# Kernel optimization log

Measured on AMD Instinct MI355X. Metric: run time of the kernel, lower is better.

The kernel has to match this reference:

```python
import jax, jax.numpy as jnp
import numpy as np

NUM_ENTITIES = 100000
NUM_RELATIONS = 500
D = 256            # embedding_dim
T = 4              # num_hash_tables
H = 32             # hash_dim
B = 64             # batch of queries
K = 10
CAND = max(K * 10, int(NUM_ENTITIES * 0.1))  # = 10000


def setup_inputs() -> dict:
    key = jax.random.key(0)
    k0, k1, k2, k3, k4 = jax.random.split(key, 5)
    return {
        "head": jax.random.randint(k0, (B,), 0, NUM_ENTITIES),
        "relation": jax.random.randint(k1, (B,), 0, NUM_RELATIONS),
        "entity_emb": jax.random.normal(k2, (NUM_ENTITIES, D), jnp.float32) * 0.02,
        "relation_emb": jax.random.normal(k3, (NUM_RELATIONS, D), jnp.float32) * 0.02,
        "hash_proj": jax.random.normal(k4, (T, D, H), jnp.float32),
        "k": K,
    }


def reference(head, relation, entity_emb, relation_emb, hash_proj, k):
    # DistMult approximate query path of KnowledgeGraph.query (use_approximate=True).
    h = entity_emb[head]            # [B, D]
    r = relation_emb[relation]      # [B, D]
    target = h * r                  # DistMult target embedding [B, D]

    # LSH hash codes (0/1 floats): projected > 0
    thash = (jnp.einsum('bd,tdh->bth', target, hash_proj) > 0).astype(jnp.float32)      # [B,T,H]
    ahash = (jnp.einsum('nd,tdh->nth', entity_emb, hash_proj) > 0).astype(jnp.float32)  # [N,T,H]

    # Hamming distance over (T,H) bits without materializing [B,N,T,H]:
    # mismatches = sum(a) + sum(b) - 2 * <a,b>  for 0/1 codes
    dot = jnp.einsum('bth,nth->bn', thash, ahash)                                        # [B,N]
    hash_dist = thash.sum((1, 2))[:, None] + ahash.sum((1, 2))[None, :] - 2.0 * dot      # [B,N]

    # top num_candidates with SMALLEST hamming distance
    _, cand_idx = jax.lax.top_k(-hash_dist, CAND)                                        # [B,CAND]

    # DistMult score: (h*r*t).sum(-1) == target . t ; compute dense then gather candidates
    scores_all = jnp.einsum('bd,nd->bn', target, entity_emb)                             # [B,N]
    cand_scores = jnp.take_along_axis(scores_all, cand_idx, axis=1)                      # [B,CAND]

    top_scores, top_local = jax.lax.top_k(cand_scores, k)                                # [B,k]
    top_indices = jnp.take_along_axis(cand_idx, top_local, axis=1)                       # [B,k]
    return top_indices, top_scores
```

## Files before the change

### kernel.cpp

```cpp
#include <hip/hip_runtime.h>
#include <hip/hip_bf16.h>
#include <float.h>

constexpr int NENT  = 100000;
constexpr int DDIM  = 256;
constexpr int BQ    = 64;
constexpr int CANDN = 10000;
constexpr int KTOP  = 10;
constexpr int NSLICE = 16;
constexpr int SLICE  = 6272;
constexpr int HPAD   = 132;

typedef short v8s __attribute__((ext_vector_type(8)));
typedef float v4f __attribute__((ext_vector_type(4)));

__device__ inline void split3(float x, unsigned short& h0, unsigned short& h1,
                              unsigned short& h2) {
    unsigned t0 = __float_as_uint(x) & 0xffff0000u;
    float r1 = x - __uint_as_float(t0);
    unsigned t1 = __float_as_uint(r1) & 0xffff0000u;
    float r2 = r1 - __uint_as_float(t1);
    h0 = (unsigned short)(t0 >> 16);
    h1 = (unsigned short)(t1 >> 16);
    h2 = (unsigned short)(__float_as_uint(r2) >> 16);
}

__device__ inline void split8p(const float* p0, const float* p1,
                               v8s& o0, v8s& o1, v8s& o2) {
    union { v8s v; unsigned short u[8]; } r0, r1, r2;
    float4 f0 = *(const float4*)p0;
    float4 f1 = *(const float4*)(p1);
    float av[8] = {f0.x, f0.y, f0.z, f0.w, f1.x, f1.y, f1.z, f1.w};
    #pragma unroll
    for (int j = 0; j < 8; j++)
        split3(av[j], r0.u[j], r1.u[j], r2.u[j]);
    o0 = r0.v; o1 = r1.v; o2 = r2.v;
}

__device__ inline void stage16(const float* g, float* l) {
    __builtin_amdgcn_global_load_lds(
        (const __attribute__((address_space(1))) void*)g,
        (__attribute__((address_space(3))) void*)l, 16, 0, 0);
}

__global__ __launch_bounds__(128) void k_targets(
    const int* __restrict__ head, const int* __restrict__ rel,
    const float* __restrict__ E, const float* __restrict__ Rm,
    const float* __restrict__ proj,
    float* __restrict__ tgtT, unsigned* __restrict__ thash)
{
    __shared__ float tg[DDIM];
    int b = blockIdx.x;
    int tid = threadIdx.x;
    int h = head[b], r = rel[b];
    for (int d = tid; d < DDIM; d += 128) {
        float v = E[h*DDIM + d] * Rm[r*DDIM + d];
        tg[d] = v;
        tgtT[d*BQ + b] = v;
    }
    __syncthreads();
    int t = tid >> 5, hh = tid & 31;
    float acc = 0.f;
    #pragma unroll 8
    for (int d = 0; d < DDIM; d++)
        acc += tg[d] * proj[(t*DDIM + d)*32 + hh];
    unsigned long long m = __ballot(acc > 0.0f);
    int lane = tid & 63, w = tid >> 6;
    if (lane == 0) {
        thash[b*4 + w*2 + 0] = (unsigned)(m & 0xffffffffull);
        thash[b*4 + w*2 + 1] = (unsigned)(m >> 32);
    }
}

__global__ __launch_bounds__(256) void k_prepw(
    const float* __restrict__ proj, const float* __restrict__ tgtT,
    unsigned short* __restrict__ Whi, unsigned short* __restrict__ Wmid,
    unsigned short* __restrict__ Wlo)
{
    int c = blockIdx.x;
    int d = threadIdx.x;
    float x = (c < 128) ? proj[((c >> 5)*DDIM + d)*32 + (c & 31)]
                        : tgtT[d*BQ + (c - 128)];
    unsigned short h0, h1, h2;
    split3(x, h0, h1, h2);
    Whi [c*DDIM + d] = h0;
    Wmid[c*DDIM + d] = h1;
    Wlo [c*DDIM + d] = h2;
}

constexpr int TILE_E = 128;

__global__ __launch_bounds__(256, 2) void k_gemm(
    const float* __restrict__ E,
    const unsigned short* __restrict__ Whi, const unsigned short* __restrict__ Wmid,
    const unsigned short* __restrict__ Wlo,
    unsigned* __restrict__ ahash, float* __restrict__ scores)
{
    __shared__ __align__(16) float Af[2][TILE_E*32];
    unsigned short* bitsHalf = (unsigned short*)Af;

    int tid = threadIdx.x;
    int l = tid & 63, w = tid >> 6;
    int wm = w >> 1, wn = w & 1;
    int m = l & 15, quad = l >> 4;
    int n0 = blockIdx.x * TILE_E;

    const float* gsrc[4];
    #pragma unroll
    for (int it = 0; it < 4; it++) {
        int U = it*256 + tid;
        int row = U >> 3;
        int us  = (U & 7) ^ (row & 7);
        int n = n0 + row; if (n >= NENT) n = NENT - 1;
        gsrc[it] = E + (size_t)n*DDIM + us*4;
    }

    int offA0[4], offA1[4];
    #pragma unroll
    for (int a = 0; a < 4; a++) {
        int row = wm*64 + a*16 + m;
        offA0[a] = row*32 + (((2*quad)    ) ^ (m & 7))*4;
        offA1[a] = row*32 + (((2*quad) | 1) ^ (m & 7))*4;
    }

    int colOff[6];
    #pragma unroll
    for (int c = 0; c < 6; c++)
        colOff[c] = (wn*96 + c*16 + m)*DDIM + quad*8;

    v4f acc[4][6];
    #pragma unroll
    for (int a = 0; a < 4; a++)
        #pragma unroll
        for (int c = 0; c < 6; c++)
            acc[a][c] = (v4f)0.0f;

    #pragma unroll
    for (int it = 0; it < 4; it++)
        stage16(gsrc[it], &Af[0][(it*256 + w*64)*4]);
    __syncthreads();

    int bb = 0;
    for (int ch = 0; ch < DDIM/32; ch++) {
        if (ch + 1 < DDIM/32) {
            const float* gadd = (const float*)((const char*)0) ; (void)gadd;
            #pragma unroll
            for (int it = 0; it < 4; it++)
                stage16(gsrc[it] + (ch + 1)*32, &Af[bb ^ 1][(it*256 + w*64)*4]);
        }

        v8s a0[4], a1[4], a2[4];
        #pragma unroll
        for (int a = 0; a < 4; a++)
            split8p(&Af[bb][offA0[a]], &Af[bb][offA1[a]], a0[a], a1[a], a2[a]);

        int d0 = ch*32;
        #pragma unroll
        for (int c = 0; c < 6; c++) {
            int co = colOff[c] + d0;
            v8s b0 = *(const v8s*)(Whi  + co);
            v8s b1 = *(const v8s*)(Wmid + co);
            v8s b2 = *(const v8s*)(Wlo  + co);
            #pragma unroll
            for (int a = 0; a < 4; a++) {
                acc[a][c] = __builtin_amdgcn_mfma_f32_16x16x32_bf16(a2[a], b0, acc[a][c], 0, 0, 0);
                acc[a][c] = __builtin_amdgcn_mfma_f32_16x16x32_bf16(a0[a], b2, acc[a][c], 0, 0, 0);
                acc[a][c] = __builtin_amdgcn_mfma_f32_16x16x32_bf16(a1[a], b1, acc[a][c], 0, 0, 0);
                acc[a][c] = __builtin_amdgcn_mfma_f32_16x16x32_bf16(a1[a], b0, acc[a][c], 0, 0, 0);
                acc[a][c] = __builtin_amdgcn_mfma_f32_16x16x32_bf16(a0[a], b1, acc[a][c], 0, 0, 0);
                acc[a][c] = __builtin_amdgcn_mfma_f32_16x16x32_bf16(a0[a], b0, acc[a][c], 0, 0, 0);
            }
        }
        __syncthreads();
        bb ^= 1;
    }

    #pragma unroll
    for (int c = 0; c < 6; c++) {
        int ct = wn*6 + c;
        if (ct < 8) {
            #pragma unroll
            for (int a = 0; a < 4; a++) {
                #pragma unroll
                for (int r = 0; r < 4; r++) {
                    unsigned long long mb = __ballot(acc[a][c][r] > 0.0f);
                    if (m == 0) {
                        int rowl = wm*64 + a*16 + quad*4 + r;
                        bitsHalf[rowl*8 + ct] = (unsigned short)(mb >> (quad*16));
                    }
                }
            }
        } else {
            int b = ct*16 - 128 + m;
            #pragma unroll
            for (int a = 0; a < 4; a++) {
                int nb = n0 + wm*64 + a*16 + quad*4;
                if (nb < NENT)
                    *(float4*)(scores + (size_t)b*NENT + nb) = *(float4*)&acc[a][c];
            }
        }
    }
    __syncthreads();
    if (tid < TILE_E) {
        int n = n0 + tid;
        if (n < NENT)
            *(uint4*)(ahash + (size_t)n*4) = *(const uint4*)&bitsHalf[tid*8];
    }
}

__global__ __launch_bounds__(256) void k_dist(
    const unsigned* __restrict__ ahash, const unsigned* __restrict__ thash,
    unsigned char* __restrict__ dist8, unsigned short* __restrict__ histG)
{
    __shared__ unsigned hist[4][HPAD];
    int s = blockIdx.x, b = blockIdx.y, tid = threadIdx.x;
    int wv = tid >> 6;
    for (int i = tid; i < 4*HPAD; i += 256) ((unsigned*)hist)[i] = 0u;
    uint4 tw = *(const uint4*)(thash + b*4);
    __syncthreads();
    int n0 = s*SLICE;
    int n1 = n0 + SLICE; if (n1 > NENT) n1 = NENT;
    unsigned char* drow = dist8 + (size_t)b*NENT;
    for (int n = n0 + tid*4; n < n1; n += 1024) {
        int dv[4];
        #pragma unroll
        for (int i = 0; i < 4; i++) {
            uint4 a = *(const uint4*)(ahash + (size_t)(n+i)*4);
            dv[i] = __popc(a.x^tw.x) + __popc(a.y^tw.y) +
                    __popc(a.z^tw.z) + __popc(a.w^tw.w);
            atomicAdd(&hist[wv][dv[i]], 1u);
        }
        uchar4 o = make_uchar4((unsigned char)dv[0], (unsigned char)dv[1],
                               (unsigned char)dv[2], (unsigned char)dv[3]);
        *(uchar4*)(drow + n) = o;
    }
    __syncthreads();
    unsigned short* hrow = histG + ((size_t)b*NSLICE + s)*HPAD;
    for (int i = tid; i < 129; i += 256)
        hrow[i] = (unsigned short)(hist[0][i] + hist[1][i] + hist[2][i] + hist[3][i]);
}

__global__ __launch_bounds__(64) void k_cut(
    const unsigned char* __restrict__ dist8, const unsigned short* __restrict__ histG,
    int* __restrict__ dsG, int* __restrict__ ncG)
{
    __shared__ unsigned histT[HPAD];
    __shared__ int dsS, slS, rpS;
    int b = blockIdx.x, tid = threadIdx.x;
    for (int d = tid; d < 129; d += 64) {
        unsigned sum = 0;
        for (int s = 0; s < NSLICE; s++)
            sum += histG[((size_t)b*NSLICE + s)*HPAD + d];
        histT[d] = sum;
    }
    __syncthreads();
    if (tid == 0) {
        unsigned cum = 0; int ds = 128; unsigned R = 1;
        for (int d = 0; d < 129; d++) {
            unsigned c = cum + histT[d];
            if (c >= (unsigned)CANDN) { ds = d; R = (unsigned)CANDN - cum; break; }
            cum = c;
        }
        dsS = ds; dsG[b] = ds;
        unsigned acc = 0;
        for (int s = 0; s < NSLICE; s++) {
            unsigned c = histG[((size_t)b*NSLICE + s)*HPAD + ds];
            if (acc + c >= R) { slS = s; rpS = (int)(R - acc); break; }
            acc += c;
        }
    }
    __syncthreads();
    int ds = dsS;
    unsigned Rp = (unsigned)rpS;
    const unsigned char* drow = dist8 + (size_t)b*NENT;
    int sBase = slS*SLICE;
    int sEnd = sBase + SLICE; if (sEnd > NENT) sEnd = NENT;
    unsigned cnt = 0;
    for (int base = sBase; base < sEnd; base += 64) {
        int n = base + tid;
        bool eq = (n < sEnd) && (drow[n] == (unsigned char)ds);
        unsigned long long mm = __ballot(eq);
        unsigned c = __popcll(mm);
        if (cnt + c >= Rp) {
            unsigned pre = __popcll(mm & ((1ull << tid) - 1ull));
            if (eq && (cnt + pre + 1u == Rp)) ncG[b] = n;
            break;
        }
        cnt += c;
    }
}

__global__ __launch_bounds__(256) void k_part(
    const unsigned char* __restrict__ dist8, const float* __restrict__ scores,
    const int* __restrict__ dsG, const int* __restrict__ ncG,
    const float* __restrict__ tgtT, const float* __restrict__ E,
    float* __restrict__ partS, int* __restrict__ partI)
{
    __shared__ float rs[256];
    __shared__ int   ri[256];
    __shared__ int   rt[256];
    __shared__ int   chosenI[KTOP];
    __shared__ float tgl[DDIM];

    int sl = blockIdx.x, b = blockIdx.y, tid = threadIdx.x;
    int ds = dsG[b], nc = ncG[b];
    const unsigned char* drow = dist8 + (size_t)b*NENT;
    const float* srow = scores + (size_t)b*NENT;
    int n0 = sl*SLICE;
    int n1 = n0 + SLICE; if (n1 > NENT) n1 = NENT;

    float topS[KTOP]; int topI[KTOP];
    #pragma unroll
    for (int i = 0; i < KTOP; i++) { topS[i] = -FLT_MAX; topI[i] = 0x7fffffff; }

    for (int n = n0 + tid*4; n < n1; n += 1024) {
        uchar4 dv = *(const uchar4*)(drow + n);
        unsigned char da[4] = {dv.x, dv.y, dv.z, dv.w};
        #pragma unroll
        for (int i = 0; i < 4; i++) {
            int d = da[i];
            int nn = n + i;
            if (d < ds || (d == ds && nn <= nc)) {
                float sc = srow[nn];
                if (sc > topS[KTOP-1]) {
                    int p = KTOP - 1;
                    while (p > 0 && topS[p-1] < sc) {
                        topS[p] = topS[p-1]; topI[p] = topI[p-1]; p--;
                    }
                    topS[p] = sc; topI[p] = nn;
                }
            }
        }
    }

    int ph = 0;
    for (int r = 0; r < KTOP; r++) {
        rs[tid] = topS[ph]; ri[tid] = topI[ph]; rt[tid] = tid;
        __syncthreads();
        for (int st = 128; st > 0; st >>= 1) {
            if (tid < st) {
                bool take = (rs[tid+st] > rs[tid]) ||
                            (rs[tid+st] == rs[tid] && ri[tid+st] < ri[tid]);
                if (take) { rs[tid]=rs[tid+st]; ri[tid]=ri[tid+st]; rt[tid]=rt[tid+st]; }
            }
            __syncthreads();
        }
        if (tid == 0) {
            chosenI[r] = ri[0];
            partI[((size_t)b*NSLICE + sl)*KTOP + r] = ri[0];
        }
        int winner = rt[0];
        __syncthreads();
        if (tid == winner) ph++;
        __syncthreads();
    }

    for (int d = tid; d < DDIM; d += 256) tgl[d] = tgtT[d*BQ + b];
    __syncthreads();
    if (tid < KTOP) {
        int idx = chosenI[tid];
        float sc = -FLT_MAX;
        if (idx >= 0 && idx < NENT) {
            const float* er = E + (size_t)idx*DDIM;
            float acc = 0.f;
            #pragma unroll 8
            for (int d = 0; d < DDIM; d += 4) {
                float4 v = *(const float4*)(er + d);
                acc += v.x*tgl[d+0];
                acc += v.y*tgl[d+1];
                acc += v.z*tgl[d+2];
                acc += v.w*tgl[d+3];
            }
            sc = acc;
        }
        partS[((size_t)b*NSLICE + sl)*KTOP + tid] = sc;
    }
}

__global__ __launch_bounds__(256) void k_merge(
    const float* __restrict__ partS, const int* __restrict__ partI,
    float* __restrict__ out)
{
    __shared__ float sc2[NSLICE*KTOP];
    __shared__ int   ix2[NSLICE*KTOP];
    int b = blockIdx.x, tid = threadIdx.x;
    if (tid < NSLICE*KTOP) {
        sc2[tid] = partS[(size_t)b*NSLICE*KTOP + tid];
        ix2[tid] = partI[(size_t)b*NSLICE*KTOP + tid];
    }
    __syncthreads();
    if (tid < NSLICE*KTOP) {
        float mv = sc2[tid]; int mi = ix2[tid];
        int rank = 0;
        #pragma unroll 8
        for (int i = 0; i < NSLICE*KTOP; i++) {
            float v = sc2[i]; int id = ix2[i];
            bool beats = (v > mv) ||
                         (v == mv && (id < mi || (id == mi && i < tid)));
            rank += beats ? 1 : 0;
        }
        if (rank < KTOP) {
            out[b*KTOP + rank]           = (float)mi;
            out[BQ*KTOP + b*KTOP + rank] = mv;
        }
    }
}

extern "C" void kernel_launch(void* const* d_in, const int* in_sizes, int n_in,
                              void* d_out, int out_size, void* d_ws, size_t ws_size,
                              hipStream_t stream)
{
    const int*   head = (const int*)d_in[0];
    const int*   rel  = (const int*)d_in[1];
    const float* E    = (const float*)d_in[2];
    const float* Rm   = (const float*)d_in[3];
    const float* proj = (const float*)d_in[4];

    char* ws = (char*)d_ws;
    float*          tgtT   = (float*)(ws);
    unsigned*       thash  = (unsigned*)(ws + 65536);
    unsigned*       ahash  = (unsigned*)(ws + 66560);
    float*          scores = (float*)(ws + 1666560);
    unsigned char*  dist8  = (unsigned char*)(ws + 27266560);
    int*            dsG    = (int*)(ws + 33666560);
    int*            ncG    = (int*)(ws + 33666816);
    float*          partS  = (float*)(ws + 33667072);
    int*            partI  = (int*)(ws + 33708032);
    unsigned short* histG  = (unsigned short*)(ws + 33748992);
    unsigned short* Whi    = (unsigned short*)(ws + 34019328);
    unsigned short* Wmid   = (unsigned short*)(ws + 34117632);
    unsigned short* Wlo    = (unsigned short*)(ws + 34215936);
    float*          out    = (float*)d_out;

    hipLaunchKernelGGL(k_targets, dim3(BQ), dim3(128), 0, stream,
                       head, rel, E, Rm, proj, tgtT, thash);
    hipLaunchKernelGGL(k_prepw, dim3(192), dim3(256), 0, stream,
                       proj, tgtT, Whi, Wmid, Wlo);
    hipLaunchKernelGGL(k_gemm, dim3((NENT + TILE_E - 1)/TILE_E), dim3(256), 0, stream,
                       E, Whi, Wmid, Wlo, ahash, scores);
    hipLaunchKernelGGL(k_dist, dim3(NSLICE, BQ), dim3(256), 0, stream,
                       ahash, thash, dist8, histG);
    hipLaunchKernelGGL(k_cut, dim3(BQ), dim3(64), 0, stream,
                       dist8, histG, dsG, ncG);
    hipLaunchKernelGGL(k_part, dim3(NSLICE, BQ), dim3(256), 0, stream,
                       dist8, scores, dsG, ncG, tgtT, E, partS, partI);
    hipLaunchKernelGGL(k_merge, dim3(BQ), dim3(256), 0, stream,
                       partS, partI, out);
}
```

Measured before the change: 347.5 us.

## Fuse prep kernels, widen histogram privatization, batch cut scan, replace iterative top-k reduction

Merges the target-embedding/hash kernel and the weight-split kernel into one launch, removing a launch and a dependency. The distance histogram is privatized per 32-lane group instead of per wavefront, which cuts atomic contention. The cut search loads four 64-element chunks before ballot-counting them. The per-slice top-10 merge, which ran ten tree reductions each with many barriers, becomes a rank-count threshold selection plus a small rank sort. The new selection logic is intricate and carries tie-handling risk.

```diff
diff --git a/kernel.cpp b/kernel.cpp
--- a/kernel.cpp
+++ b/kernel.cpp
@@ -43,49 +43,53 @@
         (__attribute__((address_space(3))) void*)l, 16, 0, 0);
 }
 
-__global__ __launch_bounds__(128) void k_targets(
+__global__ __launch_bounds__(256) void k_prep(
     const int* __restrict__ head, const int* __restrict__ rel,
     const float* __restrict__ E, const float* __restrict__ Rm,
     const float* __restrict__ proj,
-    float* __restrict__ tgtT, unsigned* __restrict__ thash)
+    float* __restrict__ tgtT, unsigned* __restrict__ thash,
+    unsigned short* __restrict__ Whi, unsigned short* __restrict__ Wmid,
+    unsigned short* __restrict__ Wlo)
 {
     __shared__ float tg[DDIM];
-    int b = blockIdx.x;
+    int blk = blockIdx.x;
     int tid = threadIdx.x;
-    int h = head[b], r = rel[b];
-    for (int d = tid; d < DDIM; d += 128) {
+    if (blk < 128) {
+        int c = blk, d = tid;
+        float x = proj[((c >> 5)*DDIM + d)*32 + (c & 31)];
+        unsigned short h0, h1, h2;
+        split3(x, h0, h1, h2);
+        Whi [c*DDIM + d] = h0;
+        Wmid[c*DDIM + d] = h1;
+        Wlo [c*DDIM + d] = h2;
+    } else {
+        int b = blk - 128;
+        int h = head[b], r = rel[b];
+        int d = tid;
         float v = E[h*DDIM + d] * Rm[r*DDIM + d];
         tg[d] = v;
         tgtT[d*BQ + b] = v;
-    }
-    __syncthreads();
-    int t = tid >> 5, hh = tid & 31;
-    float acc = 0.f;
-    #pragma unroll 8
-    for (int d = 0; d < DDIM; d++)
-        acc += tg[d] * proj[(t*DDIM + d)*32 + hh];
-    unsigned long long m = __ballot(acc > 0.0f);
-    int lane = tid & 63, w = tid >> 6;
-    if (lane == 0) {
-        thash[b*4 + w*2 + 0] = (unsigned)(m & 0xffffffffull);
-        thash[b*4 + w*2 + 1] = (unsigned)(m >> 32);
-    }
-}
-
-__global__ __launch_bounds__(256) void k_prepw(
-    const float* __restrict__ proj, const float* __restrict__ tgtT,
-    unsigned short* __restrict__ Whi, unsigned short* __restrict__ Wmid,
-    unsigned short* __restrict__ Wlo)
-{
-    int c = blockIdx.x;
-    int d = threadIdx.x;
-    float x = (c < 128) ? proj[((c >> 5)*DDIM + d)*32 + (c & 31)]
-                        : tgtT[d*BQ + (c - 128)];
-    unsigned short h0, h1, h2;
-    split3(x, h0, h1, h2);
-    Whi [c*DDIM + d] = h0;
-    Wmid[c*DDIM + d] = h1;
-    Wlo [c*DDIM + d] = h2;
+        unsigned short h0, h1, h2;
+        split3(v, h0, h1, h2);
+        int c = 128 + b;
+        Whi [c*DDIM + d] = h0;
+        Wmid[c*DDIM + d] = h1;
+        Wlo [c*DDIM + d] = h2;
+        __syncthreads();
+        if (tid < 128) {
+            int t = tid >> 5, hh = tid & 31;
+            float acc = 0.f;
+            #pragma unroll 8
+            for (int dd = 0; dd < DDIM; dd++)
+                acc += tg[dd] * proj[(t*DDIM + dd)*32 + hh];
+            unsigned long long m = __ballot(acc > 0.0f);
+            int lane = tid & 63, w = tid >> 6;
+            if (lane == 0) {
+                thash[b*4 + w*2 + 0] = (unsigned)(m & 0xffffffffull);
+                thash[b*4 + w*2 + 1] = (unsigned)(m >> 32);
+            }
+        }
+    }
 }
 
 constexpr int TILE_E = 128;
@@ -143,7 +147,6 @@
     int bb = 0;
     for (int ch = 0; ch < DDIM/32; ch++) {
         if (ch + 1 < DDIM/32) {
-            const float* gadd = (const float*)((const char*)0) ; (void)gadd;
             #pragma unroll
             for (int it = 0; it < 4; it++)
                 stage16(gsrc[it] + (ch + 1)*32, &Af[bb ^ 1][(it*256 + w*64)*4]);
@@ -212,10 +215,10 @@
     const unsigned* __restrict__ ahash, const unsigned* __restrict__ thash,
     unsigned char* __restrict__ dist8, unsigned short* __restrict__ histG)
 {
-    __shared__ unsigned hist[4][HPAD];
+    __shared__ unsigned hist[8][HPAD];
     int s = blockIdx.x, b = blockIdx.y, tid = threadIdx.x;
-    int wv = tid >> 6;
-    for (int i = tid; i < 4*HPAD; i += 256) ((unsigned*)hist)[i] = 0u;
+    int wv = tid >> 5;
+    for (int i = tid; i < 8*HPAD; i += 256) ((unsigned*)hist)[i] = 0u;
     uint4 tw = *(const uint4*)(thash + b*4);
     __syncthreads();
     int n0 = s*SLICE;
@@ -236,8 +239,12 @@
     }
     __syncthreads();
     unsigned short* hrow = histG + ((size_t)b*NSLICE + s)*HPAD;
-    for (int i = tid; i < 129; i += 256)
-        hrow[i] = (unsigned short)(hist[0][i] + hist[1][i] + hist[2][i] + hist[3][i]);
+    for (int i = tid; i < 129; i += 256) {
+        unsigned t = 0;
+        #pragma unroll
+        for (int v = 0; v < 8; v++) t += hist[v][i];
+        hrow[i] = (unsigned short)t;
+    }
 }
 
 __global__ __launch_bounds__(64) void k_cut(
@@ -276,17 +283,27 @@
     int sBase = slS*SLICE;
     int sEnd = sBase + SLICE; if (sEnd > NENT) sEnd = NENT;
     unsigned cnt = 0;
-    for (int base = sBase; base < sEnd; base += 64) {
-        int n = base + tid;
-        bool eq = (n < sEnd) && (drow[n] == (unsigned char)ds);
-        unsigned long long mm = __ballot(eq);
-        unsigned c = __popcll(mm);
-        if (cnt + c >= Rp) {
-            unsigned pre = __popcll(mm & ((1ull << tid) - 1ull));
-            if (eq && (cnt + pre + 1u == Rp)) ncG[b] = n;
-            break;
-        }
-        cnt += c;
+    for (int base = sBase; base < sEnd; base += 256) {
+        unsigned char qa[4];
+        #pragma unroll
+        for (int s4 = 0; s4 < 4; s4++) {
+            int n = base + s4*64 + tid;
+            qa[s4] = (n < sEnd) ? drow[n] : (unsigned char)255;
+        }
+        bool done = false;
+        #pragma unroll
+        for (int s4 = 0; s4 < 4; s4++) {
+            bool eq = (qa[s4] == (unsigned char)ds);
+            unsigned long long mm = __ballot(eq);
+            unsigned c = __popcll(mm);
+            if (cnt + c >= Rp) {
+                unsigned pre = __popcll(mm & ((1ull << tid) - 1ull));
+                if (eq && (cnt + pre + 1u == Rp)) ncG[b] = base + s4*64 + tid;
+                done = true; break;
+            }
+            cnt += c;
+        }
+        if (done) break;
     }
 }
 
@@ -296,9 +313,12 @@
     const float* __restrict__ tgtT, const float* __restrict__ E,
     float* __restrict__ partS, int* __restrict__ partI)
 {
-    __shared__ float rs[256];
-    __shared__ int   ri[256];
-    __shared__ int   rt[256];
+    __shared__ float ls[256];
+    __shared__ int   li[256];
+    __shared__ float ps[112];
+    __shared__ int   pi[112];
+    __shared__ int   pcnt;
+    __shared__ float TsS; __shared__ int TiS;
     __shared__ int   chosenI[KTOP];
     __shared__ float tgl[DDIM];
 
@@ -333,26 +353,46 @@
         }
     }
 
-    int ph = 0;
-    for (int r = 0; r < KTOP; r++) {
-        rs[tid] = topS[ph]; ri[tid] = topI[ph]; rt[tid] = tid;
-        __syncthreads();
-        for (int st = 128; st > 0; st >>= 1) {
-            if (tid < st) {
-                bool take = (rs[tid+st] > rs[tid]) ||
-                            (rs[tid+st] == rs[tid] && ri[tid+st] < ri[tid]);
-                if (take) { rs[tid]=rs[tid+st]; ri[tid]=ri[tid+st]; rt[tid]=rt[tid+st]; }
-            }
-            __syncthreads();
-        }
-        if (tid == 0) {
-            chosenI[r] = ri[0];
-            partI[((size_t)b*NSLICE + sl)*KTOP + r] = ri[0];
-        }
-        int winner = rt[0];
-        __syncthreads();
-        if (tid == winner) ph++;
-        __syncthreads();
+    ls[tid] = topS[0]; li[tid] = topI[0];
+    if (tid == 0) pcnt = 0;
+    if (tid < 112) { ps[tid] = -FLT_MAX; pi[tid] = 0x7fffffff; }
+    __syncthreads();
+
+    float mv = topS[0]; int mi = topI[0];
+    int rank = 0;
+    for (int i = 0; i < 256; i++) {
+        float v = ls[i]; int id = li[i];
+        rank += (v > mv || (v == mv && id < mi)) ? 1 : 0;
+    }
+    if (rank == 9 || (rank < 9 && mi == 0x7fffffff)) { TsS = mv; TiS = mi; }
+    __syncthreads();
+    float ts = TsS; int ti = TiS;
+
+    if (!(ts > mv || (ts == mv && ti < mi))) {
+        #pragma unroll
+        for (int j = 0; j < KTOP; j++) {
+            float sj = topS[j]; int ij = topI[j];
+            if (ij == 0x7fffffff) break;
+            if (sj > ts || (sj == ts && ij <= ti)) {
+                int p = atomicAdd(&pcnt, 1);
+                ps[p] = sj; pi[p] = ij;
+            } else break;
+        }
+    }
+    __syncthreads();
+
+    if (tid < 112) {
+        float s = ps[tid]; int id = pi[tid];
+        int r = 0;
+        for (int i = 0; i < 112; i++) {
+            float v = ps[i]; int iv = pi[i];
+            bool beats = (v > s) || (v == s && (iv < id || (iv == id && i < tid)));
+            r += beats ? 1 : 0;
+        }
+        if (r < KTOP) {
+            chosenI[r] = id;
+            partI[((size_t)b*NSLICE + sl)*KTOP + r] = id;
+        }
     }
 
     for (int d = tid; d < DDIM; d += 256) tgl[d] = tgtT[d*BQ + b];
@@ -432,10 +472,8 @@
     unsigned short* Wlo    = (unsigned short*)(ws + 34215936);
     float*          out    = (float*)d_out;
 
-    hipLaunchKernelGGL(k_targets, dim3(BQ), dim3(128), 0, stream,
-                       head, rel, E, Rm, proj, tgtT, thash);
-    hipLaunchKernelGGL(k_prepw, dim3(192), dim3(256), 0, stream,
-                       proj, tgtT, Whi, Wmid, Wlo);
+    hipLaunchKernelGGL(k_prep, dim3(192), dim3(256), 0, stream,
+                       head, rel, E, Rm, proj, tgtT, thash, Whi, Wmid, Wlo);
     hipLaunchKernelGGL(k_gemm, dim3((NENT + TILE_E - 1)/TILE_E), dim3(256), 0, stream,
                        E, Whi, Wmid, Wlo, ahash, scores);
     hipLaunchKernelGGL(k_dist, dim3(NSLICE, BQ), dim3(256), 0, stream,
```

Result: faster. 322.6 us (-7.2%).
